# Optimization experiments

Measured on AMD Instinct MI355X. Metric: run time of the kernel, lower is better.

The kernel has to match this reference:

```python
import jax, jax.numpy as jnp
import numpy as np

D_MODEL = 512
D_QK = 512
H = 8
HEAD_DIM = D_QK // H   # 64
V_DIM = D_MODEL // H   # 64
PROJ_OUT = D_MODEL + 2 * D_QK + H  # 1544


def setup_inputs() -> dict:
    key = jax.random.key(0)
    k1, k2, k3, k4, k5 = jax.random.split(key, 5)
    B, S = 2, 2048
    x = jax.random.normal(k1, (B, S, D_MODEL), dtype=jnp.float32)
    s_in = 1.0 / np.sqrt(D_MODEL)
    Wvqkn_w = jax.random.uniform(k2, (PROJ_OUT, D_MODEL), jnp.float32, -s_in, s_in)
    Wvqkn_b = jax.random.uniform(k3, (PROJ_OUT,), jnp.float32, -s_in, s_in)
    out_w = jax.random.uniform(k4, (D_MODEL, D_MODEL), jnp.float32, -s_in, s_in)
    out_b = jax.random.uniform(k5, (D_MODEL,), jnp.float32, -s_in, s_in)
    return {"x": x, "Wvqkn_w": Wvqkn_w, "Wvqkn_b": Wvqkn_b,
            "out_w": out_w, "out_b": out_b}


def reference(x, Wvqkn_w, Wvqkn_b, out_w, out_b):
    B, S, _ = x.shape
    # fused qkvn projection
    vqkn = jnp.einsum('bsd,od->bso', x, Wvqkn_w) + Wvqkn_b  # [B,S,1544]
    v = vqkn[..., :D_MODEL]                                  # [B,S,512]
    qk = vqkn[..., D_MODEL:D_MODEL + 2 * D_QK]               # [B,S,1024]
    n = vqkn[..., D_MODEL + 2 * D_QK:]                       # [B,S,H]
    qk = qk.reshape(B, S, 2, H, HEAD_DIM)
    v = v.reshape(B, S, H, V_DIM)
    q, k = qk[:, :, 0], qk[:, :, 1]                          # approx_fn = identity
    # linear attention via cumulative KV state (scale=1.0, scale_B=False)
    kv = jnp.einsum('bshd,bsht->bshdt', k, v)                # [B,S,H,D,Dv]
    kv = jnp.cumsum(kv, axis=1)
    out = jnp.einsum('bshd,bshdt->bsht', q, kv)              # [B,S,H,Dv]
    # normalization gating: norm_fn = exp, no offset
    gate = jnp.exp(-jnp.exp(n))                              # [B,S,H]
    ctx = gate[..., None] * out
    ctx = ctx.reshape(B, S, D_MODEL)
    return jnp.einsum('bsd,od->bso', ctx, out_w) + out_b
```

## Files before the change

### kernel.cpp

```cpp
#include <hip/hip_runtime.h>
#include <hip/hip_bf16.h>
#include <math.h>

#define B_    2
#define S_    2048
#define DM    512
#define H_    8
#define PROJ  1544
#define NPAD1 1664
#define CHK   64
#define NC    32
#define BS_   4096
#define BH    16

typedef __attribute__((ext_vector_type(8))) short shortx8;
typedef __attribute__((ext_vector_type(4))) short shortx4;
typedef __attribute__((ext_vector_type(4))) float floatx4;

#define GCAST(p) ((const __attribute__((address_space(1))) void*)(p))
#define LCAST(p) ((__attribute__((address_space(3))) void*)(p))

__device__ inline short f2bf(float f) {
    __hip_bfloat16 h = __float2bfloat16(f);
    return *(short*)&h;
}
__device__ inline float bf2f(short s) {
    __hip_bfloat16 h = *(__hip_bfloat16*)&s;
    return __bfloat162float(h);
}
__device__ inline shortx8 read8(const short* buf, int row, int k) {
    return *(const shortx8*)&buf[row * 64 + ((((k >> 3) ^ (row & 7))) << 3)];
}

#define E1 ((size_t)BS_ * DM)
#define E2 ((size_t)NPAD1 * DM)
#define E3 ((size_t)DM * DM)
__global__ __launch_bounds__(256) void convert_all(const float* __restrict__ x,
                                                   const float* __restrict__ w1,
                                                   const float* __restrict__ w2,
                                                   short* __restrict__ xb,
                                                   short* __restrict__ w1b,
                                                   short* __restrict__ w2b) {
    size_t e = ((size_t)blockIdx.x * 256 + threadIdx.x) * 8;
    const float* src;
    short* dst;
    bool zero = false;
    if (e < E1) { src = x + e; dst = xb + e; }
    else if (e < E1 + E2) {
        size_t o = e - E1;
        dst = w1b + o;
        size_t row = o >> 9;
        if (row < PROJ) src = w1 + o; else { src = w1; zero = true; }
    } else if (e < E1 + E2 + E3) {
        size_t o = e - E1 - E2;
        src = w2 + o; dst = w2b + o;
    } else return;
    short out[8];
    if (zero) {
#pragma unroll
        for (int i = 0; i < 8; i++) out[i] = 0;
    } else {
        float4 f0 = *(const float4*)src;
        float4 f1 = *(const float4*)(src + 4);
        out[0] = f2bf(f0.x); out[1] = f2bf(f0.y); out[2] = f2bf(f0.z); out[3] = f2bf(f0.w);
        out[4] = f2bf(f1.x); out[5] = f2bf(f1.y); out[6] = f2bf(f1.z); out[7] = f2bf(f1.w);
    }
    *(shortx8*)dst = *(shortx8*)out;
}

__global__ __launch_bounds__(256) void gemm_mfma64(const short* __restrict__ A,
                                                   const short* __restrict__ Bw,
                                                   const float* __restrict__ bias,
                                                   float* __restrict__ C,
                                                   int N, int K) {
    __shared__ short As[64 * 32];
    __shared__ short Bs[128 * 32];
    const int tid  = threadIdx.x;
    const int wave = tid >> 6, lane = tid & 63;
    const int m0 = blockIdx.y * 64;
    const int n0 = blockIdx.x * 128;
    const int srow  = lane >> 2;
    const int skoff = (lane & 3) * 8;
    const int lm = lane & 15, q = lane >> 4;
    const int wc = wave * 32;
    floatx4 acc[4][2] = {};

    const short* gA  = A  + (size_t)(m0 + wave * 16 + srow) * K + skoff;
    const short* gB0 = Bw + (size_t)(n0 + wave * 16 + srow) * K + skoff;
    const short* gB1 = Bw + (size_t)(n0 + 64 + wave * 16 + srow) * K + skoff;

    for (int k0 = 0; k0 < K; k0 += 32) {
        __builtin_amdgcn_global_load_lds(GCAST(gA  + k0), LCAST(&As[wave * 512]),        16, 0, 0);
        __builtin_amdgcn_global_load_lds(GCAST(gB0 + k0), LCAST(&Bs[wave * 512]),        16, 0, 0);
        __builtin_amdgcn_global_load_lds(GCAST(gB1 + k0), LCAST(&Bs[2048 + wave * 512]), 16, 0, 0);
        __syncthreads();
        shortx8 af[4], bw[2];
#pragma unroll
        for (int i = 0; i < 4; i++)
            af[i] = *(const shortx8*)&As[(i * 16 + lm) * 32 + q * 8];
#pragma unroll
        for (int j = 0; j < 2; j++)
            bw[j] = *(const shortx8*)&Bs[(wc + j * 16 + lm) * 32 + q * 8];
#pragma unroll
        for (int i = 0; i < 4; i++)
#pragma unroll
            for (int j = 0; j < 2; j++)
                acc[i][j] = __builtin_amdgcn_mfma_f32_16x16x32_bf16(af[i], bw[j], acc[i][j], 0, 0, 0);
        __syncthreads();
    }
#pragma unroll
    for (int i = 0; i < 4; i++) {
        int rb = m0 + i * 16 + q * 4;
#pragma unroll
        for (int j = 0; j < 2; j++) {
            int col = n0 + wc + j * 16 + lm;
            float bv = bias[col];
#pragma unroll
            for (int r = 0; r < 4; r++)
                C[(size_t)(rb + r) * N + col] = acc[i][j][r] + bv;
        }
    }
}

__global__ __launch_bounds__(256) void gemm1_fused(const short* __restrict__ A,
                                                   const short* __restrict__ Bw,
                                                   const float* __restrict__ bias,
                                                   short* __restrict__ qb,
                                                   short* __restrict__ kb,
                                                   short* __restrict__ kTb,
                                                   short* __restrict__ vTb,
                                                   float* __restrict__ gateb) {
    __shared__ short As[64 * 32];
    __shared__ short Bs[128 * 32];
    const int K = DM;
    const int tid  = threadIdx.x;
    const int wave = tid >> 6, lane = tid & 63;
    const int m0 = blockIdx.y * 64;
    const int n0 = blockIdx.x * 128;
    const int srow  = lane >> 2;
    const int skoff = (lane & 3) * 8;
    const int lm = lane & 15, q = lane >> 4;
    const int wc = wave * 32;
    floatx4 acc[4][2] = {};

    const short* gA  = A  + (size_t)(m0 + wave * 16 + srow) * K + skoff;
    const short* gB0 = Bw + (size_t)(n0 + wave * 16 + srow) * K + skoff;
    const short* gB1 = Bw + (size_t)(n0 + 64 + wave * 16 + srow) * K + skoff;

    for (int k0 = 0; k0 < K; k0 += 32) {
        __builtin_amdgcn_global_load_lds(GCAST(gA  + k0), LCAST(&As[wave * 512]),        16, 0, 0);
        __builtin_amdgcn_global_load_lds(GCAST(gB0 + k0), LCAST(&Bs[wave * 512]),        16, 0, 0);
        __builtin_amdgcn_global_load_lds(GCAST(gB1 + k0), LCAST(&Bs[2048 + wave * 512]), 16, 0, 0);
        __syncthreads();
        shortx8 af[4], bw[2];
#pragma unroll
        for (int i = 0; i < 4; i++)
            af[i] = *(const shortx8*)&As[(i * 16 + lm) * 32 + q * 8];
#pragma unroll
        for (int j = 0; j < 2; j++)
            bw[j] = *(const shortx8*)&Bs[(wc + j * 16 + lm) * 32 + q * 8];
#pragma unroll
        for (int i = 0; i < 4; i++)
#pragma unroll
            for (int j = 0; j < 2; j++)
                acc[i][j] = __builtin_amdgcn_mfma_f32_16x16x32_bf16(af[i], bw[j], acc[i][j], 0, 0, 0);
        __syncthreads();
    }

    const int bIdx = m0 >> 11;
    const int bh0  = bIdx * H_;
#pragma unroll
    for (int i = 0; i < 4; i++) {
        int s0 = (m0 & (S_ - 1)) + i * 16 + q * 4;
#pragma unroll
        for (int j = 0; j < 2; j++) {
            int col = n0 + wc + j * 16 + lm;
            float bv = (col < PROJ) ? bias[col] : 0.f;
            float vals[4];
#pragma unroll
            for (int r = 0; r < 4; r++) vals[r] = acc[i][j][r] + bv;
            if (col < 512) {
                int h = col >> 6, vd = col & 63;
                short tmp[4];
#pragma unroll
                for (int r = 0; r < 4; r++) tmp[r] = f2bf(vals[r]);
                *(shortx4*)&vTb[((size_t)(bh0 + h) * 64 + vd) * S_ + s0] = *(shortx4*)tmp;
            } else if (col < 1024) {
                int h = (col >> 6) - 8, d = col & 63;
                size_t rb = ((size_t)(bh0 + h) * S_ + s0) * 64 + d;
#pragma unroll
                for (int r = 0; r < 4; r++) qb[rb + (size_t)r * 64] = f2bf(vals[r]);
            } else if (col < 1536) {
                int h = (col >> 6) - 16, d = col & 63;
                size_t rb = ((size_t)(bh0 + h) * S_ + s0) * 64 + d;
                short tmp[4];
#pragma unroll
                for (int r = 0; r < 4; r++) { tmp[r] = f2bf(vals[r]); kb[rb + (size_t)r * 64] = tmp[r]; }
                *(shortx4*)&kTb[((size_t)(bh0 + h) * 64 + d) * S_ + s0] = *(shortx4*)tmp;
            } else if (col < PROJ) {
                int h = col - 1536;
                float g[4];
#pragma unroll
                for (int r = 0; r < 4; r++) g[r] = __expf(-__expf(vals[r]));
                *(float4*)&gateb[(size_t)(bh0 + h) * S_ + s0] = make_float4(g[0], g[1], g[2], g[3]);
            }
        }
    }
}

__global__ __launch_bounds__(256) void chunk_kv_mfma(const short* __restrict__ vTb,
                                                     const short* __restrict__ kTb,
                                                     float* __restrict__ kvbuf) {
    __shared__ __align__(16) short VT[64 * 64];
    __shared__ __align__(16) short KT[64 * 64];
    const int blk = blockIdx.x;
    const int c = blk & (NC - 1), bh = blk >> 5;
    const int base = c * CHK;
    const int tid = threadIdx.x, wave = tid >> 6, lane = tid & 63;
    const int lrow = lane >> 3, lgrp = lane & 7;

#pragma unroll
    for (int half = 0; half < 2; half++) {
        int v0 = wave * 8 + half * 32;
        int row = v0 + lrow;
        int gcol = ((lgrp ^ (row & 7)) << 3);
        __builtin_amdgcn_global_load_lds(GCAST(vTb + ((size_t)(bh * 64 + row)) * S_ + base + gcol),
                                         LCAST(&VT[v0 * 64]), 16, 0, 0);
        __builtin_amdgcn_global_load_lds(GCAST(kTb + ((size_t)(bh * 64 + row)) * S_ + base + gcol),
                                         LCAST(&KT[v0 * 64]), 16, 0, 0);
    }
    __syncthreads();

    const int lm = lane & 15, q = lane >> 4;
    const int wr = (wave >> 1) * 32, wc = (wave & 1) * 32;
    floatx4 acc[2][2] = {};
#pragma unroll
    for (int ks = 0; ks < 2; ks++) {
        shortx8 a[2], b2[2];
#pragma unroll
        for (int i = 0; i < 2; i++) a[i]  = read8(VT, wr + i * 16 + lm, ks * 32 + q * 8);
#pragma unroll
        for (int j = 0; j < 2; j++) b2[j] = read8(KT, wc + j * 16 + lm, ks * 32 + q * 8);
#pragma unroll
        for (int i = 0; i < 2; i++)
#pragma unroll
            for (int j = 0; j < 2; j++)
                acc[i][j] = __builtin_amdgcn_mfma_f32_16x16x32_bf16(a[i], b2[j], acc[i][j], 0, 0, 0);
    }
    float* outp = kvbuf + ((size_t)blk << 12);
#pragma unroll
    for (int i = 0; i < 2; i++)
#pragma unroll
        for (int j = 0; j < 2; j++)
#pragma unroll
            for (int r = 0; r < 4; r++)
                outp[(wr + i * 16 + q * 4 + r) * 64 + wc + j * 16 + lm] = acc[i][j][r];
}

__global__ __launch_bounds__(256) void attn_mfma(const short* __restrict__ qb,
                                                 const short* __restrict__ kb,
                                                 const short* __restrict__ vTb,
                                                 const float* __restrict__ gateb,
                                                 const float* __restrict__ kvbuf,
                                                 short* __restrict__ ctxb) {
    __shared__ __align__(16) short Qs[64 * 64];
    __shared__ __align__(16) short Ks[64 * 64];
    __shared__ __align__(16) short VTs[64 * 64];
    __shared__ __align__(16) short Phi[64 * 64];
    __shared__ __align__(16) short Plo[64 * 64];
    __shared__ __align__(16) short Sb[64 * 72];
    __shared__ float gs[64];
    const int blk = blockIdx.x;
    const int bh = blk & (BH - 1);
    const int c  = (NC - 1) - (blk >> 4);
    const int base = c * CHK;
    const int tid = threadIdx.x, wave = tid >> 6, lane = tid & 63;
    const int lrow = lane >> 3, lgrp = lane & 7;

#pragma unroll
    for (int half = 0; half < 2; half++) {
        int v0 = wave * 8 + half * 32;
        int row = v0 + lrow;
        int gcol = ((lgrp ^ (row & 7)) << 3);
        __builtin_amdgcn_global_load_lds(GCAST(qb + ((size_t)bh * S_ + base + row) * 64 + gcol),
                                         LCAST(&Qs[v0 * 64]), 16, 0, 0);
        __builtin_amdgcn_global_load_lds(GCAST(kb + ((size_t)bh * S_ + base + row) * 64 + gcol),
                                         LCAST(&Ks[v0 * 64]), 16, 0, 0);
        __builtin_amdgcn_global_load_lds(GCAST(vTb + ((size_t)(bh * 64 + row)) * S_ + base + gcol),
                                         LCAST(&VTs[v0 * 64]), 16, 0, 0);
    }

    float pacc[16] = {};
    {
        const float* kvb = kvbuf + (((size_t)bh * NC) << 12) + tid;
        for (int cp = 0; cp < c; cp++) {
            const float* p = kvb + ((size_t)cp << 12);
#pragma unroll
            for (int it = 0; it < 16; it++) pacc[it] += p[it * 256];
        }
    }
#pragma unroll
    for (int it = 0; it < 16; it++) {
        int idx = it * 256 + tid;
        int v = idx >> 6, d = idx & 63;
        float f = pacc[it];
        short hi = f2bf(f);
        short lo = f2bf(f - bf2f(hi));
        int sw = v * 64 + (((d >> 3) ^ (v & 7)) << 3) + (d & 7);
        Phi[sw] = hi; Plo[sw] = lo;
    }
    if (tid < 64) gs[tid] = gateb[(size_t)bh * S_ + base + tid];
    __syncthreads();

    const int lm = lane & 15, q = lane >> 4;
    const int wr = (wave >> 1) * 32, wc = (wave & 1) * 32;

    floatx4 sacc[2][2] = {};
#pragma unroll
    for (int ks = 0; ks < 2; ks++) {
        shortx8 qa[2], kf[2];
#pragma unroll
        for (int i = 0; i < 2; i++) qa[i] = read8(Qs, wr + i * 16 + lm, ks * 32 + q * 8);
#pragma unroll
        for (int j = 0; j < 2; j++) kf[j] = read8(Ks, wc + j * 16 + lm, ks * 32 + q * 8);
#pragma unroll
        for (int i = 0; i < 2; i++)
#pragma unroll
            for (int j = 0; j < 2; j++)
                sacc[i][j] = __builtin_amdgcn_mfma_f32_16x16x32_bf16(qa[i], kf[j], sacc[i][j], 0, 0, 0);
    }
#pragma unroll
    for (int i = 0; i < 2; i++)
#pragma unroll
        for (int j = 0; j < 2; j++)
#pragma unroll
            for (int r = 0; r < 4; r++) {
                int s = wr + i * 16 + q * 4 + r;
                int t = wc + j * 16 + lm;
                Sb[s * 72 + t] = f2bf(t <= s ? sacc[i][j][r] : 0.f);
            }
    __syncthreads();

    floatx4 oacc[2][2] = {};
#pragma unroll
    for (int ks = 0; ks < 2; ks++) {
        shortx8 sa[2], vb[2];
#pragma unroll
        for (int i = 0; i < 2; i++)
            sa[i] = *(const shortx8*)&Sb[(wr + i * 16 + lm) * 72 + ks * 32 + q * 8];
#pragma unroll
        for (int j = 0; j < 2; j++) vb[j] = read8(VTs, wc + j * 16 + lm, ks * 32 + q * 8);
#pragma unroll
        for (int i = 0; i < 2; i++)
#pragma unroll
            for (int j = 0; j < 2; j++)
                oacc[i][j] = __builtin_amdgcn_mfma_f32_16x16x32_bf16(sa[i], vb[j], oacc[i][j], 0, 0, 0);
    }
#pragma unroll
    for (int ks = 0; ks < 2; ks++) {
        shortx8 qa[2], ph[2], pl[2];
#pragma unroll
        for (int i = 0; i < 2; i++) qa[i] = read8(Qs, wr + i * 16 + lm, ks * 32 + q * 8);
#pragma unroll
        for (int j = 0; j < 2; j++) {
            ph[j] = read8(Phi, wc + j * 16 + lm, ks * 32 + q * 8);
            pl[j] = read8(Plo, wc + j * 16 + lm, ks * 32 + q * 8);
        }
#pragma unroll
        for (int i = 0; i < 2; i++)
#pragma unroll
            for (int j = 0; j < 2; j++) {
                oacc[i][j] = __builtin_amdgcn_mfma_f32_16x16x32_bf16(qa[i], ph[j], oacc[i][j], 0, 0, 0);
                oacc[i][j] = __builtin_amdgcn_mfma_f32_16x16x32_bf16(qa[i], pl[j], oacc[i][j], 0, 0, 0);
            }
    }
    const size_t tok0 = (size_t)(bh >> 3) * S_ + base;
    const int h = bh & 7;
#pragma unroll
    for (int i = 0; i < 2; i++)
#pragma unroll
        for (int j = 0; j < 2; j++)
#pragma unroll
            for (int r = 0; r < 4; r++) {
                int s = wr + i * 16 + q * 4 + r;
                int v = wc + j * 16 + lm;
                ctxb[(tok0 + s) * DM + h * 64 + v] = f2bf(gs[s] * oacc[i][j][r]);
            }
}

extern "C" void kernel_launch(void* const* d_in, const int* in_sizes, int n_in,
                              void* d_out, int out_size, void* d_ws, size_t ws_size,
                              hipStream_t stream) {
    const float* x       = (const float*)d_in[0];
    const float* Wvqkn_w = (const float*)d_in[1];
    const float* Wvqkn_b = (const float*)d_in[2];
    const float* out_w   = (const float*)d_in[3];
    const float* out_b   = (const float*)d_in[4];
    float* out = (float*)d_out;

    float* kvbuf = (float*)d_ws;
    short* xb    = (short*)(kvbuf + (size_t)BH * NC * 4096);
    short* w1b   = xb   + (size_t)BS_ * DM;
    short* w2b   = w1b  + (size_t)NPAD1 * DM;
    short* ctxb  = w2b  + (size_t)DM * DM;
    short* qb    = ctxb + (size_t)BS_ * DM;
    short* kb    = qb   + (size_t)BH * S_ * 64;
    short* kTb   = kb   + (size_t)BH * S_ * 64;
    short* vTb   = kTb  + (size_t)BH * S_ * 64;
    float* gateb = (float*)(vTb + (size_t)BH * S_ * 64);

    convert_all<<<(int)((E1 + E2 + E3) / 8 / 256), 256, 0, stream>>>(
        x, Wvqkn_w, out_w, xb, w1b, w2b);

    gemm1_fused<<<dim3(NPAD1 / 128, BS_ / 64), 256, 0, stream>>>(
        xb, w1b, Wvqkn_b, qb, kb, kTb, vTb, gateb);

    chunk_kv_mfma<<<BH * NC, 256, 0, stream>>>(vTb, kTb, kvbuf);
    attn_mfma<<<BH * NC, 256, 0, stream>>>(qb, kb, vTb, gateb, kvbuf, ctxb);

    gemm_mfma64<<<dim3(DM / 128, BS_ / 64), 256, 0, stream>>>(ctxb, w2b, out_b, out, DM, DM);
}
```

Before: 121.2 us.

## Widen GEMM K-tile with swizzled LDS and add grouped KV prefix scan

Both GEMM kernels now stage 64-wide K tiles instead of 32, using an XOR-swizzled LDS layout read through read8. This halves the number of barrier-separated iterations and issues more MFMAs per sync. A new scan_groups kernel precomputes exclusive prefix sums of the chunk KV states at every 4-chunk boundary. The attention kernel then starts from that group prefix and adds at most 3 chunks, instead of summing up to 31 chunk states serially. The cost is an extra kernel launch, extra workspace, and doubled LDS per GEMM block, which may reduce occupancy.

```diff
diff --git a/kernel.cpp b/kernel.cpp
--- a/kernel.cpp
+++ b/kernel.cpp
@@ -73,39 +73,47 @@
                                                    const float* __restrict__ bias,
                                                    float* __restrict__ C,
                                                    int N, int K) {
-    __shared__ short As[64 * 32];
-    __shared__ short Bs[128 * 32];
+    __shared__ __align__(16) short As[64 * 64];
+    __shared__ __align__(16) short Bs[128 * 64];
     const int tid  = threadIdx.x;
     const int wave = tid >> 6, lane = tid & 63;
     const int m0 = blockIdx.y * 64;
     const int n0 = blockIdx.x * 128;
-    const int srow  = lane >> 2;
-    const int skoff = (lane & 3) * 8;
+    const int lrow = lane >> 3;
+    const int swz  = ((lane & 7) ^ lrow) << 3;
     const int lm = lane & 15, q = lane >> 4;
     const int wc = wave * 32;
     floatx4 acc[4][2] = {};
 
-    const short* gA  = A  + (size_t)(m0 + wave * 16 + srow) * K + skoff;
-    const short* gB0 = Bw + (size_t)(n0 + wave * 16 + srow) * K + skoff;
-    const short* gB1 = Bw + (size_t)(n0 + 64 + wave * 16 + srow) * K + skoff;
-
-    for (int k0 = 0; k0 < K; k0 += 32) {
-        __builtin_amdgcn_global_load_lds(GCAST(gA  + k0), LCAST(&As[wave * 512]),        16, 0, 0);
-        __builtin_amdgcn_global_load_lds(GCAST(gB0 + k0), LCAST(&Bs[wave * 512]),        16, 0, 0);
-        __builtin_amdgcn_global_load_lds(GCAST(gB1 + k0), LCAST(&Bs[2048 + wave * 512]), 16, 0, 0);
+    const short* gA0 = A  + (size_t)(m0 +      wave * 8 + lrow) * K + swz;
+    const short* gA1 = A  + (size_t)(m0 + 32 + wave * 8 + lrow) * K + swz;
+    const short* gB[4];
+#pragma unroll
+    for (int h = 0; h < 4; h++)
+        gB[h] = Bw + (size_t)(n0 + h * 32 + wave * 8 + lrow) * K + swz;
+
+    for (int k0 = 0; k0 < K; k0 += 64) {
+        __builtin_amdgcn_global_load_lds(GCAST(gA0 + k0), LCAST(&As[(wave * 8) * 64]),        16, 0, 0);
+        __builtin_amdgcn_global_load_lds(GCAST(gA1 + k0), LCAST(&As[(32 + wave * 8) * 64]),   16, 0, 0);
+#pragma unroll
+        for (int h = 0; h < 4; h++)
+            __builtin_amdgcn_global_load_lds(GCAST(gB[h] + k0), LCAST(&Bs[(h * 32 + wave * 8) * 64]), 16, 0, 0);
         __syncthreads();
-        shortx8 af[4], bw[2];
-#pragma unroll
-        for (int i = 0; i < 4; i++)
-            af[i] = *(const shortx8*)&As[(i * 16 + lm) * 32 + q * 8];
-#pragma unroll
-        for (int j = 0; j < 2; j++)
-            bw[j] = *(const shortx8*)&Bs[(wc + j * 16 + lm) * 32 + q * 8];
-#pragma unroll
-        for (int i = 0; i < 4; i++)
-#pragma unroll
-            for (int j = 0; j < 2; j++)
-                acc[i][j] = __builtin_amdgcn_mfma_f32_16x16x32_bf16(af[i], bw[j], acc[i][j], 0, 0, 0);
+        shortx8 af[2][4], bw[2][2];
+#pragma unroll
+        for (int ks = 0; ks < 2; ks++) {
+#pragma unroll
+            for (int i = 0; i < 4; i++) af[ks][i] = read8(As, i * 16 + lm, ks * 32 + q * 8);
+#pragma unroll
+            for (int j = 0; j < 2; j++) bw[ks][j] = read8(Bs, wc + j * 16 + lm, ks * 32 + q * 8);
+        }
+#pragma unroll
+        for (int ks = 0; ks < 2; ks++)
+#pragma unroll
+            for (int i = 0; i < 4; i++)
+#pragma unroll
+                for (int j = 0; j < 2; j++)
+                    acc[i][j] = __builtin_amdgcn_mfma_f32_16x16x32_bf16(af[ks][i], bw[ks][j], acc[i][j], 0, 0, 0);
         __syncthreads();
     }
 #pragma unroll
@@ -130,40 +138,48 @@
                                                    short* __restrict__ kTb,
                                                    short* __restrict__ vTb,
                                                    float* __restrict__ gateb) {
-    __shared__ short As[64 * 32];
-    __shared__ short Bs[128 * 32];
+    __shared__ __align__(16) short As[64 * 64];
+    __shared__ __align__(16) short Bs[128 * 64];
     const int K = DM;
     const int tid  = threadIdx.x;
     const int wave = tid >> 6, lane = tid & 63;
     const int m0 = blockIdx.y * 64;
     const int n0 = blockIdx.x * 128;
-    const int srow  = lane >> 2;
-    const int skoff = (lane & 3) * 8;
+    const int lrow = lane >> 3;
+    const int swz  = ((lane & 7) ^ lrow) << 3;
     const int lm = lane & 15, q = lane >> 4;
     const int wc = wave * 32;
     floatx4 acc[4][2] = {};
 
-    const short* gA  = A  + (size_t)(m0 + wave * 16 + srow) * K + skoff;
-    const short* gB0 = Bw + (size_t)(n0 + wave * 16 + srow) * K + skoff;
-    const short* gB1 = Bw + (size_t)(n0 + 64 + wave * 16 + srow) * K + skoff;
-
-    for (int k0 = 0; k0 < K; k0 += 32) {
-        __builtin_amdgcn_global_load_lds(GCAST(gA  + k0), LCAST(&As[wave * 512]),        16, 0, 0);
-        __builtin_amdgcn_global_load_lds(GCAST(gB0 + k0), LCAST(&Bs[wave * 512]),        16, 0, 0);
-        __builtin_amdgcn_global_load_lds(GCAST(gB1 + k0), LCAST(&Bs[2048 + wave * 512]), 16, 0, 0);
+    const short* gA0 = A  + (size_t)(m0 +      wave * 8 + lrow) * K + swz;
+    const short* gA1 = A  + (size_t)(m0 + 32 + wave * 8 + lrow) * K + swz;
+    const short* gB[4];
+#pragma unroll
+    for (int h = 0; h < 4; h++)
+        gB[h] = Bw + (size_t)(n0 + h * 32 + wave * 8 + lrow) * K + swz;
+
+    for (int k0 = 0; k0 < K; k0 += 64) {
+        __builtin_amdgcn_global_load_lds(GCAST(gA0 + k0), LCAST(&As[(wave * 8) * 64]),        16, 0, 0);
+        __builtin_amdgcn_global_load_lds(GCAST(gA1 + k0), LCAST(&As[(32 + wave * 8) * 64]),   16, 0, 0);
+#pragma unroll
+        for (int h = 0; h < 4; h++)
+            __builtin_amdgcn_global_load_lds(GCAST(gB[h] + k0), LCAST(&Bs[(h * 32 + wave * 8) * 64]), 16, 0, 0);
         __syncthreads();
-        shortx8 af[4], bw[2];
-#pragma unroll
-        for (int i = 0; i < 4; i++)
-            af[i] = *(const shortx8*)&As[(i * 16 + lm) * 32 + q * 8];
-#pragma unroll
-        for (int j = 0; j < 2; j++)
-            bw[j] = *(const shortx8*)&Bs[(wc + j * 16 + lm) * 32 + q * 8];
-#pragma unroll
-        for (int i = 0; i < 4; i++)
-#pragma unroll
-            for (int j = 0; j < 2; j++)
-                acc[i][j] = __builtin_amdgcn_mfma_f32_16x16x32_bf16(af[i], bw[j], acc[i][j], 0, 0, 0);
+        shortx8 af[2][4], bw[2][2];
+#pragma unroll
+        for (int ks = 0; ks < 2; ks++) {
+#pragma unroll
+            for (int i = 0; i < 4; i++) af[ks][i] = read8(As, i * 16 + lm, ks * 32 + q * 8);
+#pragma unroll
+            for (int j = 0; j < 2; j++) bw[ks][j] = read8(Bs, wc + j * 16 + lm, ks * 32 + q * 8);
+        }
+#pragma unroll
+        for (int ks = 0; ks < 2; ks++)
+#pragma unroll
+            for (int i = 0; i < 4; i++)
+#pragma unroll
+                for (int j = 0; j < 2; j++)
+                    acc[i][j] = __builtin_amdgcn_mfma_f32_16x16x32_bf16(af[ks][i], bw[ks][j], acc[i][j], 0, 0, 0);
         __syncthreads();
     }
 
@@ -257,11 +273,29 @@
                 outp[(wr + i * 16 + q * 4 + r) * 64 + wc + j * 16 + lm] = acc[i][j][r];
 }
 
+__global__ __launch_bounds__(256) void scan_groups(const float* __restrict__ kvbuf,
+                                                   float* __restrict__ kvg) {
+    const int blk = blockIdx.x;
+    const int bh = blk >> 4, seg = blk & 15;
+    const int e = seg * 256 + threadIdx.x;
+    const float* src = kvbuf + (((size_t)bh * NC) << 12) + e;
+    float* dst = kvg + (((size_t)bh * 8) << 12) + e;
+    float run = 0.f;
+#pragma unroll
+    for (int g = 0; g < 8; g++) {
+        dst[(size_t)g << 12] = run;
+#pragma unroll
+        for (int cc = 0; cc < 4; cc++)
+            run += src[(size_t)(g * 4 + cc) << 12];
+    }
+}
+
 __global__ __launch_bounds__(256) void attn_mfma(const short* __restrict__ qb,
                                                  const short* __restrict__ kb,
                                                  const short* __restrict__ vTb,
                                                  const float* __restrict__ gateb,
                                                  const float* __restrict__ kvbuf,
+                                                 const float* __restrict__ kvg,
                                                  short* __restrict__ ctxb) {
     __shared__ __align__(16) short Qs[64 * 64];
     __shared__ __align__(16) short Ks[64 * 64];
@@ -290,10 +324,13 @@
                                          LCAST(&VTs[v0 * 64]), 16, 0, 0);
     }
 
-    float pacc[16] = {};
+    float pacc[16];
     {
+        const float* gp = kvg + (((size_t)bh * 8 + (c >> 2)) << 12) + tid;
+#pragma unroll
+        for (int it = 0; it < 16; it++) pacc[it] = gp[it * 256];
         const float* kvb = kvbuf + (((size_t)bh * NC) << 12) + tid;
-        for (int cp = 0; cp < c; cp++) {
+        for (int cp = c & ~3; cp < c; cp++) {
             const float* p = kvb + ((size_t)cp << 12);
 #pragma unroll
             for (int it = 0; it < 16; it++) pacc[it] += p[it * 256];
@@ -399,7 +436,8 @@
     float* out = (float*)d_out;
 
     float* kvbuf = (float*)d_ws;
-    short* xb    = (short*)(kvbuf + (size_t)BH * NC * 4096);
+    float* kvg   = kvbuf + (size_t)BH * NC * 4096;
+    short* xb    = (short*)(kvg + (size_t)BH * 8 * 4096);
     short* w1b   = xb   + (size_t)BS_ * DM;
     short* w2b   = w1b  + (size_t)NPAD1 * DM;
     short* ctxb  = w2b  + (size_t)DM * DM;
@@ -416,7 +454,8 @@
         xb, w1b, Wvqkn_b, qb, kb, kTb, vTb, gateb);
 
     chunk_kv_mfma<<<BH * NC, 256, 0, stream>>>(vTb, kTb, kvbuf);
-    attn_mfma<<<BH * NC, 256, 0, stream>>>(qb, kb, vTb, gateb, kvbuf, ctxb);
+    scan_groups<<<BH * 16, 256, 0, stream>>>(kvbuf, kvg);
+    attn_mfma<<<BH * NC, 256, 0, stream>>>(qb, kb, vTb, gateb, kvbuf, kvg, ctxb);
 
     gemm_mfma64<<<dim3(DM / 128, BS_ / 64), 256, 0, stream>>>(ctxb, w2b, out_b, out, DM, DM);
 }
```

Result: faster. 109.7 us (-9.5%).
